# Kernel tuning notes

Measured on AMD Instinct MI355X. Metric: run time of the kernel, lower is better.

## Reference

```python
import jax, jax.numpy as jnp
import numpy as np

B, N, C, H = 16, 577, 768, 12
D = C // H
BETA = 1.0
KEEP_RATIO = 0.5


def setup_inputs() -> dict:
    key = jax.random.key(0)
    k0, k1, k2, k3 = jax.random.split(key, 4)
    x = jax.random.normal(k0, (B, N, C), dtype=jnp.float32)
    # UCB visit-count buffer, strictly positive as accumulated counts would be
    ucb_count_score = jax.random.uniform(k1, (H, N), dtype=jnp.float32) * 50.0 + 1.0
    Wqkv = jax.random.normal(k2, (3 * C, C), dtype=jnp.float32) * 0.02
    Wproj = jax.random.normal(k3, (C, C), dtype=jnp.float32) * 0.02
    bproj = jnp.zeros((C,), dtype=jnp.float32)
    counter = 60  # > 50 so pruning path is taken
    return {"x": x, "ucb_count_score": ucb_count_score, "Wqkv": Wqkv,
            "Wproj": Wproj, "bproj": bproj, "counter": counter}


def reference(x, ucb_count_score, Wqkv, Wproj, bproj, counter):
    # UCBAttention.forward with pruning_enabled=True, selection_mode='ucb',
    # ucb_update_enabled=True, exclude_cls=True, dropout=0 (eval).
    Bs, Ns, Cs = x.shape
    scale = D ** -0.5
    k_keep = max(1, int((Ns - 1) * KEEP_RATIO))  # _get_k with keep_ratio

    qkv = (x @ Wqkv.T).reshape(Bs, Ns, 3, H, D).transpose(2, 0, 3, 1, 4)  # [3,B,H,N,D]
    q, k, v = qkv[0], qkv[1], qkv[2]
    attn_scores = jnp.einsum('bhqd,bhkd->bhqk', q, k) * scale
    attn_probs = jax.nn.softmax(attn_scores, axis=-1)  # [B,H,N,N]

    # UCB scores over patches (CLS excluded)
    patch_scores = attn_probs[:, :, :, 1:].mean(axis=2)            # [B,H,N-1]
    expl = BETA * jnp.sqrt(jnp.log(counter + 1.0) / (ucb_count_score[:, 1:] + 1e-6))
    ucb_scores = patch_scores + expl[None, :, :]                   # [B,H,N-1]
    global_ucb = ucb_scores.mean(axis=1)                           # [B,N-1]
    _, topk_rel = jax.lax.top_k(global_ucb, k_keep)                # [B,k]
    kept = topk_rel + 1                                            # token indices

    # keep-vector: CLS (0) always kept; mask[i,j] = kept[i] OR kept[j]
    kv_mask = (jnp.zeros((Bs, Ns), attn_probs.dtype)
               .at[jnp.arange(Bs)[:, None], kept].set(1.0)
               .at[:, 0].set(1.0))                                 # [B,N]
    mask = jnp.maximum(kv_mask[:, None, :, None], kv_mask[:, None, None, :])  # [B,1,N,N]

    pruned = attn_probs * mask
    pruned = pruned / (pruned.sum(axis=-1, keepdims=True) + 1e-8)
    context = jnp.einsum('bhqk,bhkd->bhqd', pruned, v)             # [B,H,N,D]

    out = context.transpose(0, 2, 1, 3).reshape(Bs, Ns, Cs) @ Wproj.T + bproj

    # score_delta: +1/B at each kept token column, broadcast over heads
    delta = jnp.zeros((Ns,), jnp.float32).at[kept.reshape(-1)].add(1.0 / Bs)
    score_delta = jnp.broadcast_to(delta[None, :], ucb_count_score.shape)
    return out, score_delta, kept
```

## Files before the change

### kernel.cpp

```cpp
#include <hip/hip_runtime.h>
#include <cstdio>
#include <cstdint>

#define B_    16
#define N_    577
#define C_    768
#define H_    12
#define D_    64
#define KKEEP 288
#define SCALE 0.125f
#define LOG2E 1.4426950408889634f
#define M_TOT (B_ * N_)
#define NKT   24
#define PLROW ((size_t)N_ * 64)

typedef __bf16 bf16x8_t __attribute__((ext_vector_type(8)));
typedef __bf16 bf16x4_t __attribute__((ext_vector_type(4)));
typedef float  f32x4_t  __attribute__((ext_vector_type(4)));
typedef unsigned int u32x4_t __attribute__((ext_vector_type(4)));
typedef unsigned int u32x2_t __attribute__((ext_vector_type(2)));

__device__ __forceinline__ f32x4_t mfma_bf16(bf16x8_t a, bf16x8_t b, f32x4_t c) {
    return __builtin_amdgcn_mfma_f32_16x16x32_bf16(a, b, c, 0, 0, 0);
}

__device__ __forceinline__ void gload16(const ushort* g, ushort* l) {
    __builtin_amdgcn_global_load_lds(
        (const __attribute__((address_space(1))) void*)g,
        (__attribute__((address_space(3))) void*)l, 16, 0, 0);
}
#define VMCNT(n) asm volatile("s_waitcnt vmcnt(" #n ")" ::: "memory")
#define LGKM0()  asm volatile("s_waitcnt lgkmcnt(0)" ::: "memory")
#define SB() __builtin_amdgcn_sched_barrier(0)

__device__ __forceinline__ int xcd_swz(int bid, int nwg) {
    int q = nwg >> 3, r = nwg & 7;
    int xcd = bid & 7, off = bid >> 3;
    int base = (xcd < r) ? xcd * (q + 1) : r * (q + 1) + (xcd - r) * q;
    return base + off;
}

__device__ __forceinline__ void splitf(float x, unsigned int &hi, unsigned int &lo) {
    unsigned int u = __float_as_uint(x);
    hi = u >> 16;
    float r = x - __uint_as_float(u & 0xffff0000u);
    lo = __float_as_uint(r) >> 16;
}
__device__ __forceinline__ unsigned int bf16rne(float x) {
    unsigned int u = __float_as_uint(x);
    return (u + 0x7fffu + ((u >> 16) & 1u)) >> 16;
}

__global__ __launch_bounds__(256) void pack_tiles_kernel(const float* __restrict__ src,
                                                         ushort* __restrict__ dH,
                                                         ushort* __restrict__ dL,
                                                         int nrows) {
    int tile = blockIdx.x;
    int kt = tile % NKT, mt = tile / NKT;
    int w = threadIdx.x;
    int row = w >> 1, h = w & 1;
    int m = mt * 128 + row;
    int sw = (row >> 1) & 3;
    float f[16];
    if (m < nrows) {
        const float* s = src + (size_t)m * C_ + kt * 32;
        int sa = (2 * h) ^ sw, sb = (2 * h + 1) ^ sw;
        *(float4*)&f[0]  = *(const float4*)(s + sa * 8);
        *(float4*)&f[4]  = *(const float4*)(s + sa * 8 + 4);
        *(float4*)&f[8]  = *(const float4*)(s + sb * 8);
        *(float4*)&f[12] = *(const float4*)(s + sb * 8 + 4);
    } else {
#pragma unroll
        for (int i = 0; i < 16; i++) f[i] = 0.f;
    }
    unsigned hi[16], lo[16];
#pragma unroll
    for (int i = 0; i < 16; i++) splitf(f[i], hi[i], lo[i]);
    u32x4_t h0 = {hi[0] | (hi[1] << 16), hi[2] | (hi[3] << 16),
                  hi[4] | (hi[5] << 16), hi[6] | (hi[7] << 16)};
    u32x4_t h1 = {hi[8] | (hi[9] << 16), hi[10] | (hi[11] << 16),
                  hi[12] | (hi[13] << 16), hi[14] | (hi[15] << 16)};
    u32x4_t l0 = {lo[0] | (lo[1] << 16), lo[2] | (lo[3] << 16),
                  lo[4] | (lo[5] << 16), lo[6] | (lo[7] << 16)};
    u32x4_t l1 = {lo[8] | (lo[9] << 16), lo[10] | (lo[11] << 16),
                  lo[12] | (lo[13] << 16), lo[14] | (lo[15] << 16)};
    size_t dbase = (size_t)tile * 4096 + row * 32;
    *(u32x4_t*)&dH[dbase + (2 * h) * 8]     = h0;
    *(u32x4_t*)&dH[dbase + (2 * h + 1) * 8] = h1;
    *(u32x4_t*)&dL[dbase + (2 * h) * 8]     = l0;
    *(u32x4_t*)&dL[dbase + (2 * h + 1) * 8] = l1;
}

__global__ __launch_bounds__(256) void pack_rne_kernel(const float* __restrict__ src,
                                                       ushort* __restrict__ dst, int n8) {
    int i = blockIdx.x * 256 + threadIdx.x;
    if (i >= n8) return;
    float4 f0 = ((const float4*)src)[2 * i];
    float4 f1 = ((const float4*)src)[2 * i + 1];
    u32x4_t o = {bf16rne(f0.x) | (bf16rne(f0.y) << 16),
                 bf16rne(f0.z) | (bf16rne(f0.w) << 16),
                 bf16rne(f1.x) | (bf16rne(f1.y) << 16),
                 bf16rne(f1.z) | (bf16rne(f1.w) << 16)};
    *(u32x4_t*)&dst[(size_t)i * 8] = o;
}

__device__ __forceinline__ bf16x8_t fragT(const ushort* H, int row, int c, int ls) {
    int phys = ((c << 2) + ls) ^ (row & 7);
    return __builtin_bit_cast(bf16x8_t, *(const u32x4_t*)&H[(row << 6) + (phys << 3)]);
}

__global__ __launch_bounds__(256) void gemm_qk_mfma(const ushort* __restrict__ XplH,
                                                    const ushort* __restrict__ XplL,
                                                    const ushort* __restrict__ WplH,
                                                    const ushort* __restrict__ WplL,
                                                    ushort* __restrict__ qhp,
                                                    ushort* __restrict__ qlp,
                                                    ushort* __restrict__ khp,
                                                    ushort* __restrict__ klp) {
    __shared__ ushort SMEM[32768];
    ushort* Ah = SMEM;
    ushort* Al = SMEM + 8192;
    ushort* Bh = SMEM + 16384;
    ushort* Bl = SMEM + 24576;
    const int bid = xcd_swz(blockIdx.x, 12 * 73);
    const int bx = bid % 12, by = bid / 12;
    const int tid = threadIdx.x;
    const int lane = tid & 63, wave = tid >> 6;
    const int wr = wave >> 1, wc = wave & 1;
    const int lr = lane & 15, ls = lane >> 4;
    const int m0 = by * 128, n0 = bx * 128;
    const int s = n0 / C_;
    const int o0 = wave * 1024, o1 = o0 + 512;
    const int la = lane * 8;
    const size_t abase = (size_t)by * NKT * 4096;
    const size_t bbase = (size_t)bx * NKT * 4096;
    f32x4_t acc[4][4] = {};

    auto stage = [&](int buf, int kt) {
        const size_t ta = abase + (size_t)kt * 4096;
        const size_t tb = bbase + (size_t)kt * 4096;
        gload16(XplH + ta + o0 + la, &Ah[buf * 4096 + o0]);
        gload16(XplH + ta + o1 + la, &Ah[buf * 4096 + o1]);
        gload16(XplL + ta + o0 + la, &Al[buf * 4096 + o0]);
        gload16(XplL + ta + o1 + la, &Al[buf * 4096 + o1]);
        gload16(WplH + tb + o0 + la, &Bh[buf * 4096 + o0]);
        gload16(WplH + tb + o1 + la, &Bh[buf * 4096 + o1]);
        gload16(WplL + tb + o0 + la, &Bl[buf * 4096 + o0]);
        gload16(WplL + tb + o1 + la, &Bl[buf * 4096 + o1]);
    };
    stage(0, 0);
#pragma unroll 1
    for (int kt = 0; kt < NKT; ++kt) {
        const int cur = kt & 1;
        if (kt + 1 < NKT) {
            stage(cur ^ 1, kt + 1);
            VMCNT(8);
        } else {
            VMCNT(0);
        }
        SB();
        __builtin_amdgcn_s_barrier();
        SB();
        bf16x8_t fah[4], fal[4], fbh[4], fbl[4];
#pragma unroll
        for (int i = 0; i < 4; i++) {
            int rowA = wr * 64 + i * 16 + lr;
            int pa = ls ^ ((rowA >> 1) & 3);
            fah[i] = __builtin_bit_cast(bf16x8_t, *(const u32x4_t*)&Ah[cur * 4096 + rowA * 32 + pa * 8]);
            fal[i] = __builtin_bit_cast(bf16x8_t, *(const u32x4_t*)&Al[cur * 4096 + rowA * 32 + pa * 8]);
            int rowB = wc * 64 + i * 16 + lr;
            int pb = ls ^ ((rowB >> 1) & 3);
            fbh[i] = __builtin_bit_cast(bf16x8_t, *(const u32x4_t*)&Bh[cur * 4096 + rowB * 32 + pb * 8]);
            fbl[i] = __builtin_bit_cast(bf16x8_t, *(const u32x4_t*)&Bl[cur * 4096 + rowB * 32 + pb * 8]);
        }
#pragma unroll
        for (int i = 0; i < 4; i++)
#pragma unroll
            for (int j = 0; j < 4; j++) {
                acc[i][j] = mfma_bf16(fah[i], fbh[j], acc[i][j]);
                acc[i][j] = mfma_bf16(fah[i], fbl[j], acc[i][j]);
                acc[i][j] = mfma_bf16(fal[i], fbh[j], acc[i][j]);
            }
        if (kt + 1 < NKT) {
            SB();
            __builtin_amdgcn_s_barrier();
        }
    }
    __syncthreads();
    unsigned* T = (unsigned*)SMEM;
    const float sc = (s == 0) ? SCALE * LOG2E : 1.0f;
#pragma unroll
    for (int j = 0; j < 4; j++) {
        int nl = wc * 64 + j * 16 + lr;
#pragma unroll
        for (int i = 0; i < 4; i++) {
#pragma unroll
            for (int r = 0; r < 4; r++) {
                int ml = wr * 64 + i * 16 + ls * 4 + r;
                unsigned hi, lo;
                splitf(acc[i][j][r] * sc, hi, lo);
                int idx = ml * 128 + ((((nl >> 3) ^ (ml & 7)) << 3) | (nl & 7));
                T[idx] = hi | (lo << 16);
            }
        }
    }
    __syncthreads();
    ushort* dh = (s == 1) ? khp : qhp;
    ushort* dl = (s == 1) ? klp : qlp;
    const int hh0 = (n0 % C_) / D_;
#pragma unroll
    for (int it = 0; it < 8; ++it) {
        int g = it * 256 + tid;
        int sl = g & 7;
        int m_local = (g >> 3) & 127;
        int hh_half = g >> 10;
        int m = m0 + m_local;
        if (m < M_TOT) {
            int b = m / N_, n = m % N_;
            int dg = sl ^ (n & 7);
            int grp = (hh_half * 8 + dg) ^ (m_local & 7);
            const unsigned* src = &T[m_local * 128 + grp * 8];
            u32x4_t a = *(const u32x4_t*)src;
            u32x4_t bvv = *(const u32x4_t*)(src + 4);
            u32x4_t hiv = {(a[0] & 0xffffu) | (a[1] << 16),
                           (a[2] & 0xffffu) | (a[3] << 16),
                           (bvv[0] & 0xffffu) | (bvv[1] << 16),
                           (bvv[2] & 0xffffu) | (bvv[3] << 16)};
            u32x4_t lov = {(a[0] >> 16) | (a[1] & 0xffff0000u),
                           (a[2] >> 16) | (a[3] & 0xffff0000u),
                           (bvv[0] >> 16) | (bvv[1] & 0xffff0000u),
                           (bvv[2] >> 16) | (bvv[3] & 0xffff0000u)};
            size_t off = (size_t)(b * H_ + hh0 + hh_half) * PLROW + (size_t)n * 64 + sl * 8;
            *(u32x4_t*)&dh[off] = hiv;
            *(u32x4_t*)&dl[off] = lov;
        }
    }
}

__global__ __launch_bounds__(256) void gemm_v_mfma(const ushort* __restrict__ XplH,
                                                   const ushort* __restrict__ XplL,
                                                   const ushort* __restrict__ WplH,
                                                   ushort* __restrict__ vtp) {
    __shared__ ushort Ah[2][4096], Al[2][4096], Bh[2][4096];
    const int bid = xcd_swz(blockIdx.x, 6 * 73);
    const int bx = bid % 6, by = bid / 6;
    const int tid = threadIdx.x;
    const int lane = tid & 63, wave = tid >> 6;
    const int wr = wave >> 1, wc = wave & 1;
    const int lr = lane & 15, ls = lane >> 4;
    const int m0 = by * 128, n0v = bx * 128;
    const int o0 = wave * 1024, o1 = o0 + 512;
    const int la = lane * 8;
    const size_t abase = (size_t)by * NKT * 4096;
    const size_t bbase = (size_t)(12 + bx) * NKT * 4096;
    f32x4_t acc[4][4] = {};

    auto stage = [&](int buf, int kt) {
        const size_t ta = abase + (size_t)kt * 4096;
        const size_t tb = bbase + (size_t)kt * 4096;
        gload16(XplH + ta + o0 + la, &Ah[buf][o0]);
        gload16(XplH + ta + o1 + la, &Ah[buf][o1]);
        gload16(XplL + ta + o0 + la, &Al[buf][o0]);
        gload16(XplL + ta + o1 + la, &Al[buf][o1]);
        gload16(WplH + tb + o0 + la, &Bh[buf][o0]);
        gload16(WplH + tb + o1 + la, &Bh[buf][o1]);
    };
    stage(0, 0);
#pragma unroll 1
    for (int kt = 0; kt < NKT; ++kt) {
        const int cur = kt & 1;
        if (kt + 1 < NKT) {
            stage(cur ^ 1, kt + 1);
            VMCNT(6);
        } else {
            VMCNT(0);
        }
        SB();
        __builtin_amdgcn_s_barrier();
        SB();
        bf16x8_t fah[4], fal[4], fbh[4];
#pragma unroll
        for (int i = 0; i < 4; i++) {
            int rowA = wr * 64 + i * 16 + lr;
            int pa = ls ^ ((rowA >> 1) & 3);
            fah[i] = __builtin_bit_cast(bf16x8_t, *(const u32x4_t*)&Ah[cur][rowA * 32 + pa * 8]);
            fal[i] = __builtin_bit_cast(bf16x8_t, *(const u32x4_t*)&Al[cur][rowA * 32 + pa * 8]);
            int rowB = wc * 64 + i * 16 + lr;
            int pb = ls ^ ((rowB >> 1) & 3);
            fbh[i] = __builtin_bit_cast(bf16x8_t, *(const u32x4_t*)&Bh[cur][rowB * 32 + pb * 8]);
        }
#pragma unroll
        for (int i = 0; i < 4; i++)
#pragma unroll
            for (int j = 0; j < 4; j++) {
                acc[i][j] = mfma_bf16(fah[i], fbh[j], acc[i][j]);
                acc[i][j] = mfma_bf16(fal[i], fbh[j], acc[i][j]);
            }
        if (kt + 1 < NKT) {
            SB();
            __builtin_amdgcn_s_barrier();
        }
    }
#pragma unroll
    for (int j = 0; j < 4; j++) {
        int ng = n0v + wc * 64 + j * 16 + lr;
        int hh = ng / D_;
        int d = ng % D_;
#pragma unroll
        for (int i = 0; i < 4; i++) {
            int mg0 = m0 + wr * 64 + i * 16 + ls * 4;
#pragma unroll
            for (int r = 0; r < 4; r++) {
                int m = mg0 + r;
                if (m < M_TOT) {
                    int b = m / N_, n = m % N_;
                    int jt = n >> 6, jl = n & 63;
                    size_t off = ((size_t)(b * H_ + hh) * 10 + jt) * 4096 +
                                 (size_t)d * 64 + (((jl >> 3) ^ (d & 7)) << 3) + (jl & 7);
                    vtp[off] = __builtin_bit_cast(unsigned short, (__bf16)acc[i][j][r]);
                }
            }
        }
    }
}

__global__ __launch_bounds__(512) void attn_rowsum_mfma(const ushort* __restrict__ qh,
                                                        const ushort* __restrict__ ql,
                                                        const ushort* __restrict__ kh,
                                                        const ushort* __restrict__ kl,
                                                        float* __restrict__ w) {
    __shared__ ushort Qh[8192], Ql[8192];
    __shared__ ushort Kh[4096], Kl[4096];
    __shared__ float red[8][64];
    const int bid = xcd_swz(blockIdx.x, 5 * B_ * H_);
    const int bh = bid / 5, q0 = (bid % 5) * 128;
    const int tid = threadIdx.x, lane = tid & 63, wv = tid >> 6;
    const int wg = wv >> 2, wl = wv & 3;
    const int lr = lane & 15, ls = lane >> 4;
    const size_t bho = (size_t)bh * PLROW;
    const ushort* qhp = qh + bho; const ushort* qlp = ql + bho;
    const ushort* khp = kh + bho; const ushort* klp = kl + bho;
    auto qrow = [&](int rr) { return (size_t)min(q0 + wv * 16 + rr * 8 + (lane >> 3), N_ - 1) * 64 + (lane & 7) * 8; };
    gload16(qhp + qrow(0), &Qh[wv * 1024]);
    gload16(qhp + qrow(1), &Qh[wv * 1024 + 512]);
    gload16(qlp + qrow(0), &Ql[wv * 1024]);
    gload16(qlp + qrow(1), &Ql[wv * 1024 + 512]);
    auto krow = [&](int j0) { return (size_t)min(j0 + wv * 8 + (lane >> 3), N_ - 1) * 64 + (lane & 7) * 8; };
    auto stageK = [&](int j0) {
        gload16(khp + krow(j0), &Kh[wv * 512]);
        gload16(klp + krow(j0), &Kl[wv * 512]);
    };
    stageK(0);
    VMCNT(0);
    __syncthreads();
    bf16x8_t fqh[4][2], fql[4][2];
#pragma unroll
    for (int i = 0; i < 4; i++)
#pragma unroll
        for (int c = 0; c < 2; c++) {
            fqh[i][c] = fragT(Qh, wg * 64 + i * 16 + lr, c, ls);
            fql[i][c] = fragT(Ql, wg * 64 + i * 16 + lr, c, ls);
        }
    float rs[4] = {0.f, 0.f, 0.f, 0.f};
#pragma unroll 1
    for (int t = 0; t < 10; ++t) {
        bf16x8_t fkh[2], fkl[2];
#pragma unroll
        for (int c = 0; c < 2; c++) {
            fkh[c] = fragT(Kh, wl * 16 + lr, c, ls);
            fkl[c] = fragT(Kl, wl * 16 + lr, c, ls);
        }
        int jbase = t * 64 + wl * 16 + ls * 4;
#pragma unroll
        for (int i = 0; i < 4; i++) {
            f32x4_t s = {0.f, 0.f, 0.f, 0.f};
            __builtin_amdgcn_s_setprio(1);
#pragma unroll
            for (int c = 0; c < 2; c++) {
                s = mfma_bf16(fkh[c], fqh[i][c], s);
                s = mfma_bf16(fkh[c], fql[i][c], s);
                s = mfma_bf16(fkl[c], fqh[i][c], s);
            }
            __builtin_amdgcn_s_setprio(0);
#pragma unroll
            for (int r = 0; r < 4; r++)
                rs[i] += (jbase + r < N_) ? __builtin_amdgcn_exp2f(s[r]) : 0.f;
        }
        if (t < 9) {
            SB(); __builtin_amdgcn_s_barrier(); SB();
            stageK((t + 1) * 64);
            VMCNT(0);
            SB(); __builtin_amdgcn_s_barrier(); SB();
        }
    }
#pragma unroll
    for (int i = 0; i < 4; i++) {
        float v2 = rs[i];
        v2 += __shfl_xor(v2, 16);
        v2 += __shfl_xor(v2, 32);
        if (ls == 0) red[wv][i * 16 + lr] = v2;
    }
    __syncthreads();
    if (tid < 128) {
        int grp = tid >> 6, qlc = tid & 63;
        float s = red[grp * 4 + 0][qlc] + red[grp * 4 + 1][qlc] +
                  red[grp * 4 + 2][qlc] + red[grp * 4 + 3][qlc];
        int qn = q0 + tid;
        if (qn < N_) w[(size_t)bh * N_ + qn] = 1.0f / s;
    }
}

__global__ __launch_bounds__(512) void attn_colsum_mfma(const ushort* __restrict__ qh,
                                                        const ushort* __restrict__ ql,
                                                        const ushort* __restrict__ kh,
                                                        const ushort* __restrict__ kl,
                                                        const float* __restrict__ w,
                                                        float* __restrict__ colsum) {
    __shared__ ushort KhS[8192], KlS[8192];
    __shared__ ushort Qh[4096], Ql[4096];
    __shared__ float wsAll[640];
    __shared__ float red[8][64];
    const int bid = xcd_swz(blockIdx.x, 5 * B_ * H_);
    const int bh = bid / 5, j0 = (bid % 5) * 128;
    const int tid = threadIdx.x, lane = tid & 63, wv = tid >> 6;
    const int wg = wv >> 2, wl = wv & 3;
    const int lr = lane & 15, ls = lane >> 4;
    const size_t bho = (size_t)bh * PLROW;
    const ushort* qhp = qh + bho; const ushort* qlp = ql + bho;
    const ushort* khp = kh + bho; const ushort* klp = kl + bho;
    auto krow = [&](int rr) { return (size_t)min(j0 + wv * 16 + rr * 8 + (lane >> 3), N_ - 1) * 64 + (lane & 7) * 8; };
    gload16(khp + krow(0), &KhS[wv * 1024]);
    gload16(khp + krow(1), &KhS[wv * 1024 + 512]);
    gload16(klp + krow(0), &KlS[wv * 1024]);
    gload16(klp + krow(1), &KlS[wv * 1024 + 512]);
    auto qrow2 = [&](int qt) { return (size_t)min(qt + wv * 8 + (lane >> 3), N_ - 1) * 64 + (lane & 7) * 8; };
    auto stageQ = [&](int qt) {
        gload16(qhp + qrow2(qt), &Qh[wv * 512]);
        gload16(qlp + qrow2(qt), &Ql[wv * 512]);
    };
    stageQ(0);
    for (int i2 = tid; i2 < 640; i2 += 512)
        wsAll[i2] = (i2 < N_) ? w[(size_t)bh * N_ + i2] : 0.f;
    VMCNT(0);
    __syncthreads();
    bf16x8_t fkh[4][2], fkl[4][2];
#pragma unroll
    for (int i = 0; i < 4; i++)
#pragma unroll
        for (int c = 0; c < 2; c++) {
            fkh[i][c] = fragT(KhS, wg * 64 + i * 16 + lr, c, ls);
            fkl[i][c] = fragT(KlS, wg * 64 + i * 16 + lr, c, ls);
        }
    float cs[4] = {0.f, 0.f, 0.f, 0.f};
#pragma unroll 1
    for (int t = 0; t < 10; ++t) {
        bf16x8_t fqh[2], fql[2];
#pragma unroll
        for (int c = 0; c < 2; c++) {
            fqh[c] = fragT(Qh, wl * 16 + lr, c, ls);
            fql[c] = fragT(Ql, wl * 16 + lr, c, ls);
        }
        float wq[4];
#pragma unroll
        for (int r = 0; r < 4; r++) wq[r] = wsAll[t * 64 + wl * 16 + ls * 4 + r];
#pragma unroll
        for (int i = 0; i < 4; i++) {
            f32x4_t s = {0.f, 0.f, 0.f, 0.f};
            __builtin_amdgcn_s_setprio(1);
#pragma unroll
            for (int c = 0; c < 2; c++) {
                s = mfma_bf16(fqh[c], fkh[i][c], s);
                s = mfma_bf16(fql[c], fkh[i][c], s);
                s = mfma_bf16(fqh[c], fkl[i][c], s);
            }
            __builtin_amdgcn_s_setprio(0);
#pragma unroll
            for (int r = 0; r < 4; r++) cs[i] += __builtin_amdgcn_exp2f(s[r]) * wq[r];
        }
        if (t < 9) {
            SB(); __builtin_amdgcn_s_barrier(); SB();
            stageQ((t + 1) * 64);
            VMCNT(0);
            SB(); __builtin_amdgcn_s_barrier(); SB();
        }
    }
#pragma unroll
    for (int i = 0; i < 4; i++) {
        float v2 = cs[i];
        v2 += __shfl_xor(v2, 16);
        v2 += __shfl_xor(v2, 32);
        if (ls == 0) red[wv][i * 16 + lr] = v2;
    }
    __syncthreads();
    if (tid < 128) {
        int grp = tid >> 6, jlc = tid & 63;
        float t2 = red[grp * 4 + 0][jlc] + red[grp * 4 + 1][jlc] +
                   red[grp * 4 + 2][jlc] + red[grp * 4 + 3][jlc];
        int jn = j0 + tid;
        if (jn < N_) colsum[(size_t)bh * N_ + jn] = t2;
    }
}

__global__ __launch_bounds__(512) void topk_kernel(const float* __restrict__ colsum,
                                                   const float* __restrict__ ucb_count,
                                                   const int* __restrict__ counter,
                                                   float* __restrict__ kept_out,
                                                   float* __restrict__ kvmask) {
    __shared__ float sv[1024];
    __shared__ int si[1024];
    int b = blockIdx.x, tid = threadIdx.x;
    float lc = logf((float)counter[0] + 1.0f);
    for (int t = tid; t < 1024; t += 512) {
        if (t < N_ - 1) {
            int tok = t + 1;
            float accv = 0.f;
#pragma unroll
            for (int h = 0; h < H_; h++) {
                float csv = colsum[(size_t)(b * H_ + h) * N_ + tok];
                float patch = csv * (1.0f / (float)N_);
                float cnt = ucb_count[h * N_ + tok];
                float expl = sqrtf(lc / (cnt + 1e-6f));
                accv += patch + expl;
            }
            sv[t] = accv * (1.0f / (float)H_);
            si[t] = t;
        } else {
            sv[t] = -INFINITY;
            si[t] = 1 << 20;
        }
    }
    __syncthreads();
    for (int kk = 2; kk <= 1024; kk <<= 1) {
        for (int jj = kk >> 1; jj > 0; jj >>= 1) {
            for (int t = tid; t < 1024; t += 512) {
                int ixj = t ^ jj;
                if (ixj > t) {
                    float v1 = sv[t], v2 = sv[ixj];
                    int i1 = si[t], i2 = si[ixj];
                    bool before21 = (v2 > v1) || (v2 == v1 && i2 < i1);
                    bool dirDesc = ((t & kk) == 0);
                    if (before21 == dirDesc) {
                        sv[t] = v2; sv[ixj] = v1;
                        si[t] = i2; si[ixj] = i1;
                    }
                }
            }
            __syncthreads();
        }
    }
    for (int r = tid; r < KKEEP; r += 512) {
        int tok = si[r] + 1;
        kept_out[b * KKEEP + r] = (float)tok;
        kvmask[b * N_ + tok] = 1.0f;
    }
    if (tid == 0) kvmask[b * N_] = 1.0f;
}

__global__ void score_delta_kernel(const float* __restrict__ kvmask,
                                   float* __restrict__ sd) {
    int idx = blockIdx.x * 256 + threadIdx.x;
    if (idx >= H_ * N_) return;
    int n = idx % N_;
    float d = 0.f;
    if (n != 0) {
#pragma unroll
        for (int b = 0; b < B_; b++) d += kvmask[b * N_ + n];
    }
    sd[idx] = d * (1.0f / (float)B_);
}

__global__ __launch_bounds__(512) void attn_ctx_mfma(const ushort* __restrict__ qh,
                                                     const ushort* __restrict__ ql,
                                                     const ushort* __restrict__ kh,
                                                     const ushort* __restrict__ vtp,
                                                     const float* __restrict__ kvmask,
                                                     ushort* __restrict__ ctxb) {
    __shared__ ushort Kh[2][4096], Vt[2][4096];
    __shared__ ushort Pl[2][4096];
    __shared__ float mkAll[640];
    float (*red)[64] = (float(*)[64])&Pl[0][0];
    float* inv = (float*)&Pl[1][0];
    const int bid = xcd_swz(blockIdx.x, 5 * B_ * H_);
    const int bh = bid / 5, q0 = (bid % 5) * 128;
    const int b = bh / H_, h = bh % H_;
    const int tid = threadIdx.x, lane = tid & 63, wv = tid >> 6;
    const int wg = wv >> 2, wl = wv & 3;
    const int lr = lane & 15, ls = lane >> 4;
    const size_t bho = (size_t)bh * PLROW;
    const ushort* qhp = qh + bho; const ushort* qlp = ql + bho;
    const ushort* khp = kh + bho;
    const ushort* vtb = vtp + (size_t)bh * 10 * 4096;
    ushort* PlS = &Pl[0][0];
    for (int i2 = tid; i2 < 640; i2 += 512)
        mkAll[i2] = (i2 < N_) ? kvmask[(size_t)b * N_ + i2] : 0.f;
    auto qrow = [&](int rr) { return (size_t)min(q0 + wv * 16 + rr * 8 + (lane >> 3), N_ - 1) * 64 + (lane & 7) * 8; };
    bf16x8_t fqh[4][2], fql[4][2];
    gload16(qhp + qrow(0), &PlS[wv * 1024]);
    gload16(qhp + qrow(1), &PlS[wv * 1024 + 512]);
    VMCNT(0); __syncthreads();
#pragma unroll
    for (int i = 0; i < 4; i++)
#pragma unroll
        for (int c = 0; c < 2; c++)
            fqh[i][c] = fragT(PlS, wg * 64 + i * 16 + lr, c, ls);
    __syncthreads();
    gload16(qlp + qrow(0), &PlS[wv * 1024]);
    gload16(qlp + qrow(1), &PlS[wv * 1024 + 512]);
    VMCNT(0); __syncthreads();
#pragma unroll
    for (int i = 0; i < 4; i++)
#pragma unroll
        for (int c = 0; c < 2; c++)
            fql[i][c] = fragT(PlS, wg * 64 + i * 16 + lr, c, ls);
    __syncthreads();
    auto krow = [&](int j0) { return (size_t)min(j0 + wv * 8 + (lane >> 3), N_ - 1) * 64 + (lane & 7) * 8; };
    auto stageKV = [&](int buf, int t) {
        gload16(khp + krow(t * 64), &Kh[buf][wv * 512]);
        gload16(vtb + (size_t)t * 4096 + wv * 512 + lane * 8, &Vt[buf][wv * 512]);
    };
    float mq[4];
#pragma unroll
    for (int i = 0; i < 4; i++) mq[i] = mkAll[q0 + wg * 64 + i * 16 + lr];
    stageKV(0, 0);
    f32x4_t acc[4] = {};
    float psums[4] = {0.f, 0.f, 0.f, 0.f};
#pragma unroll 1
    for (int t = 0; t < 10; ++t) {
        const int cur = t & 1;
        if (t < 9) { stageKV(cur ^ 1, t + 1); VMCNT(2); }
        else      { VMCNT(0); }
        SB(); __builtin_amdgcn_s_barrier(); SB();
        bf16x8_t fkh[2];
#pragma unroll
        for (int c = 0; c < 2; c++)
            fkh[c] = fragT(Kh[cur], wl * 16 + lr, c, ls);
        int jloc = wl * 16 + ls * 4;
        float jmv[4], jbias[4];
#pragma unroll
        for (int r = 0; r < 4; r++) {
            int j = t * 64 + jloc + r;
            jmv[r] = mkAll[t * 64 + jloc + r];
            jbias[r] = (j < N_) ? 0.f : -16384.f;
        }
#pragma unroll
        for (int i = 0; i < 4; i++) {
            f32x4_t s = {0.f, 0.f, 0.f, 0.f};
            __builtin_amdgcn_s_setprio(1);
#pragma unroll
            for (int c = 0; c < 2; c++) {
                s = mfma_bf16(fkh[c], fqh[i][c], s);
                s = mfma_bf16(fkh[c], fql[i][c], s);
            }
            __builtin_amdgcn_s_setprio(0);
            bf16x4_t pb;
            float mqi = mq[i];
#pragma unroll
            for (int r = 0; r < 4; r++) {
                float p = __builtin_amdgcn_exp2f(s[r] + jbias[r]) * fmaxf(mqi, jmv[r]);
                psums[i] += p;
                pb[r] = (__bf16)p;
            }
            int row = i * 16 + lr;
            int slot = ((wl << 1) + (ls >> 1)) ^ (row & 7);
            *(u32x2_t*)&Pl[wg][(row << 6) + (slot << 3) + ((ls & 1) << 2)] =
                __builtin_bit_cast(u32x2_t, pb);
        }
        SB(); LGKM0(); SB();
        __builtin_amdgcn_s_barrier();
        SB();
        bf16x8_t fv[2];
#pragma unroll
        for (int c = 0; c < 2; c++) fv[c] = fragT(Vt[cur], wl * 16 + lr, c, ls);
        __builtin_amdgcn_s_setprio(1);
#pragma unroll
        for (int i = 0; i < 4; i++) {
            bf16x8_t fp0 = fragT(Pl[wg], i * 16 + lr, 0, ls);
            bf16x8_t fp1 = fragT(Pl[wg], i * 16 + lr, 1, ls);
            acc[i] = mfma_bf16(fv[0], fp0, acc[i]);
            acc[i] = mfma_bf16(fv[1], fp1, acc[i]);
        }
        __builtin_amdgcn_s_setprio(0);
        if (t < 9) { SB(); __builtin_amdgcn_s_barrier(); }
    }
    __syncthreads();
#pragma unroll
    for (int i = 0; i < 4; i++) {
        float v2 = psums[i];
        v2 += __shfl_xor(v2, 16);
        v2 += __shfl_xor(v2, 32);
        if (ls == 0) red[wv][i * 16 + lr] = v2;
    }
    __syncthreads();
    if (tid < 128) {
        int grp = tid >> 6, qlc = tid & 63;
        float t2 = red[grp * 4 + 0][qlc] + red[grp * 4 + 1][qlc] +
                   red[grp * 4 + 2][qlc] + red[grp * 4 + 3][qlc];
        inv[tid] = 1.0f / (t2 + 1e-8f);
    }
    __syncthreads();
#pragma unroll
    for (int i = 0; i < 4; i++) {
        int qn = q0 + wg * 64 + i * 16 + lr;
        if (qn < N_) {
            float rn = inv[wg * 64 + i * 16 + lr];
            bf16x4_t ov;
            ov[0] = (__bf16)(acc[i][0] * rn);
            ov[1] = (__bf16)(acc[i][1] * rn);
            ov[2] = (__bf16)(acc[i][2] * rn);
            ov[3] = (__bf16)(acc[i][3] * rn);
            *(u32x2_t*)&ctxb[((size_t)(b * N_ + qn)) * C_ + h * D_ + wl * 16 + ls * 4] =
                __builtin_bit_cast(u32x2_t, ov);
        }
    }
}

__global__ __launch_bounds__(256) void gemm_proj_mfma(const ushort* __restrict__ Actx,
                                                      const ushort* __restrict__ Wb,
                                                      const float* __restrict__ bias,
                                                      float* __restrict__ out) {
    __shared__ ushort Ab[128 * 32], Bb[128 * 32];
    const int bid = xcd_swz(blockIdx.x, 6 * 73);
    const int bx = bid % 6, by = bid / 6;
    const int tid = threadIdx.x;
    const int lane = tid & 63, wave = tid >> 6;
    const int wr = wave >> 1, wc = wave & 1;
    const int lr = lane & 15, ls = lane >> 4;
    const int m0 = by * 128, n0 = bx * 128;
    const int srow = tid >> 1, shalf = tid & 1;
    const int arow = min(m0 + srow, M_TOT - 1);
    const ushort* aptr = Actx + (size_t)arow * C_ + shalf * 16;
    const ushort* bptr = Wb + (size_t)(n0 + srow) * C_ + shalf * 16;
    const int swz = (srow >> 1) & 3;
    const int sidx = srow * 32;
    const int p0 = (shalf * 2 + 0) ^ swz, p1 = (shalf * 2 + 1) ^ swz;
    f32x4_t acc[4][4] = {};
#pragma unroll 1
    for (int k0 = 0; k0 < C_; k0 += 32) {
        __syncthreads();
        {
            u32x4_t c0 = *(const u32x4_t*)(aptr + k0);
            u32x4_t c1 = *(const u32x4_t*)(aptr + k0 + 8);
            *(u32x4_t*)&Ab[sidx + p0 * 8] = c0;
            *(u32x4_t*)&Ab[sidx + p1 * 8] = c1;
        }
        {
            u32x4_t c0 = *(const u32x4_t*)(bptr + k0);
            u32x4_t c1 = *(const u32x4_t*)(bptr + k0 + 8);
            *(u32x4_t*)&Bb[sidx + p0 * 8] = c0;
            *(u32x4_t*)&Bb[sidx + p1 * 8] = c1;
        }
        __syncthreads();
        bf16x8_t fa[4], fb[4];
#pragma unroll
        for (int i = 0; i < 4; i++) {
            int rowA = wr * 64 + i * 16 + lr;
            int pa = ls ^ ((rowA >> 1) & 3);
            fa[i] = __builtin_bit_cast(bf16x8_t, *(const u32x4_t*)&Ab[rowA * 32 + pa * 8]);
            int rowB = wc * 64 + i * 16 + lr;
            int pb = ls ^ ((rowB >> 1) & 3);
            fb[i] = __builtin_bit_cast(bf16x8_t, *(const u32x4_t*)&Bb[rowB * 32 + pb * 8]);
        }
#pragma unroll
        for (int i = 0; i < 4; i++)
#pragma unroll
            for (int j = 0; j < 4; j++)
                acc[i][j] = mfma_bf16(fa[i], fb[j], acc[i][j]);
    }
#pragma unroll
    for (int j = 0; j < 4; j++) {
        int ng = n0 + wc * 64 + j * 16 + lr;
        float bb = bias[ng];
#pragma unroll
        for (int i = 0; i < 4; i++) {
            int mg0 = m0 + wr * 64 + i * 16 + ls * 4;
#pragma unroll
            for (int r = 0; r < 4; r++) {
                int m = mg0 + r;
                if (m < M_TOT) out[(size_t)m * C_ + ng] = acc[i][j][r] + bb;
            }
        }
    }
}

extern "C" void kernel_launch(void* const* d_in, const int* in_sizes, int n_in,
                              void* d_out, int out_size, void* d_ws, size_t ws_size,
                              hipStream_t stream) {
    const float* x     = (const float*)d_in[0];
    const float* ucb   = (const float*)d_in[1];
    const float* Wqkv  = (const float*)d_in[2];
    const float* Wproj = (const float*)d_in[3];
    const float* bproj = (const float*)d_in[4];
    const int*   counter = (const int*)d_in[5];

    const size_t BHN  = (size_t)B_ * H_ * N_;
    const size_t XPL  = (size_t)(73 * 128) * C_;
    const size_t WPL  = (size_t)3 * C_ * C_;
    const size_t WPJ  = (size_t)C_ * C_;
    const size_t PLN  = (size_t)192 * PLROW;
    const size_t VTSZ = (size_t)192 * 10 * 4096;

    ushort* qhp  = (ushort*)d_ws;
    ushort* qlp  = qhp + PLN;
    ushort* khp  = qlp + PLN;
    ushort* klp  = khp + PLN;
    ushort* vtp  = klp + PLN;
    ushort* XplH = vtp + VTSZ;
    ushort* XplL = XplH + XPL;
    ushort* ctxb = XplH;
    ushort* WplH = XplL + XPL;
    ushort* WplL = WplH + WPL;
    ushort* Wpjb = WplL + WPL;
    float*  w    = (float*)(Wpjb + WPJ);
    float*  colsum = w + BHN;
    float*  kvmask = colsum + BHN;
    size_t need = ((char*)(kvmask + (size_t)B_ * N_)) - (char*)d_ws;
    if (ws_size < need) {
        fprintf(stderr, "kernel_launch: ws too small, need %zu have %zu\n",
                need, ws_size);
        return;
    }

    float* out  = (float*)d_out;
    float* sd   = out + (size_t)B_ * N_ * C_;
    float* kept = sd + (size_t)H_ * N_;

    hipMemsetAsync(kvmask, 0, (size_t)B_ * N_ * sizeof(float), stream);

    pack_tiles_kernel<<<73 * NKT, 256, 0, stream>>>(x, XplH, XplL, M_TOT);
    pack_tiles_kernel<<<18 * NKT, 256, 0, stream>>>(Wqkv, WplH, WplL, 3 * C_);
    pack_rne_kernel<<<(int)(WPJ / 8 / 256), 256, 0, stream>>>(Wproj, Wpjb, (int)(WPJ / 8));

    gemm_qk_mfma<<<12 * 73, 256, 0, stream>>>(XplH, XplL, WplH, WplL,
                                              qhp, qlp, khp, klp);
    gemm_v_mfma<<<6 * 73, 256, 0, stream>>>(XplH, XplL, WplH, vtp);
    attn_rowsum_mfma<<<5 * B_ * H_, 512, 0, stream>>>(qhp, qlp, khp, klp, w);
    attn_colsum_mfma<<<5 * B_ * H_, 512, 0, stream>>>(qhp, qlp, khp, klp, w, colsum);
    topk_kernel<<<B_, 512, 0, stream>>>(colsum, ucb, counter, kept, kvmask);
    score_delta_kernel<<<(H_ * N_ + 255) / 256, 256, 0, stream>>>(kvmask, sd);
    attn_ctx_mfma<<<5 * B_ * H_, 512, 0, stream>>>(qhp, qlp, khp, vtp,
                                                   kvmask, ctxb);
    gemm_proj_mfma<<<6 * 73, 256, 0, stream>>>(ctxb, Wpjb, bproj, out);
}
```

Measured before the change: 310.5 us.

## Merge pack, memset, QKV GEMMs and score-delta launches into fewer kernels

Folds the two tile-pack kernels, the Wproj bf16 pack and the kvmask memset into one pack_all kernel. The separate QK and V GEMMs become a single gemm_qkv launch that branches on the column tile, and score_delta now runs as extra blocks of attn_ctx. The aim is fewer launches and gaps between kernels, and letting the V tiles fill the GPU alongside the QK tiles. It also changes the LDS swizzle in the Q/K epilogue transpose, which may alter bank conflicts. The fused GEMM kernel carries the register and LDS needs of both paths.

```diff
diff --git a/kernel.cpp b/kernel.cpp
--- a/kernel.cpp
+++ b/kernel.cpp
@@ -51,11 +51,10 @@
     return (u + 0x7fffu + ((u >> 16) & 1u)) >> 16;
 }
 
-__global__ __launch_bounds__(256) void pack_tiles_kernel(const float* __restrict__ src,
-                                                         ushort* __restrict__ dH,
-                                                         ushort* __restrict__ dL,
-                                                         int nrows) {
-    int tile = blockIdx.x;
+__device__ __forceinline__ void pack_tile(const float* __restrict__ src,
+                                          ushort* __restrict__ dH,
+                                          ushort* __restrict__ dL,
+                                          int nrows, int tile) {
     int kt = tile % NKT, mt = tile / NKT;
     int w = threadIdx.x;
     int row = w >> 1, h = w & 1;
@@ -91,17 +90,38 @@
     *(u32x4_t*)&dL[dbase + (2 * h + 1) * 8] = l1;
 }
 
-__global__ __launch_bounds__(256) void pack_rne_kernel(const float* __restrict__ src,
-                                                       ushort* __restrict__ dst, int n8) {
-    int i = blockIdx.x * 256 + threadIdx.x;
-    if (i >= n8) return;
-    float4 f0 = ((const float4*)src)[2 * i];
-    float4 f1 = ((const float4*)src)[2 * i + 1];
-    u32x4_t o = {bf16rne(f0.x) | (bf16rne(f0.y) << 16),
-                 bf16rne(f0.z) | (bf16rne(f0.w) << 16),
-                 bf16rne(f1.x) | (bf16rne(f1.y) << 16),
-                 bf16rne(f1.z) | (bf16rne(f1.w) << 16)};
-    *(u32x4_t*)&dst[(size_t)i * 8] = o;
+#define NXP 1752
+#define NWP 432
+#define NRNE 288
+#define NZ  37
+
+__global__ __launch_bounds__(256) void pack_all_kernel(const float* __restrict__ x,
+                                                       const float* __restrict__ Wqkv,
+                                                       const float* __restrict__ Wproj,
+                                                       ushort* __restrict__ XplH,
+                                                       ushort* __restrict__ XplL,
+                                                       ushort* __restrict__ WplH,
+                                                       ushort* __restrict__ WplL,
+                                                       ushort* __restrict__ Wpjb,
+                                                       float* __restrict__ kvmask) {
+    int bid = blockIdx.x;
+    if (bid < NXP) {
+        pack_tile(x, XplH, XplL, M_TOT, bid);
+    } else if (bid < NXP + NWP) {
+        pack_tile(Wqkv, WplH, WplL, 3 * C_, bid - NXP);
+    } else if (bid < NXP + NWP + NRNE) {
+        int i = (bid - NXP - NWP) * 256 + threadIdx.x;
+        float4 f0 = ((const float4*)Wproj)[2 * i];
+        float4 f1 = ((const float4*)Wproj)[2 * i + 1];
+        u32x4_t o = {bf16rne(f0.x) | (bf16rne(f0.y) << 16),
+                     bf16rne(f0.z) | (bf16rne(f0.w) << 16),
+                     bf16rne(f1.x) | (bf16rne(f1.y) << 16),
+                     bf16rne(f1.z) | (bf16rne(f1.w) << 16)};
+        *(u32x4_t*)&Wpjb[(size_t)i * 8] = o;
+    } else {
+        int i = (bid - NXP - NWP - NRNE) * 256 + threadIdx.x;
+        if (i < B_ * N_) kvmask[i] = 0.f;
+    }
 }
 
 __device__ __forceinline__ bf16x8_t fragT(const ushort* H, int row, int c, int ls) {
@@ -109,215 +129,201 @@
     return __builtin_bit_cast(bf16x8_t, *(const u32x4_t*)&H[(row << 6) + (phys << 3)]);
 }
 
-__global__ __launch_bounds__(256) void gemm_qk_mfma(const ushort* __restrict__ XplH,
-                                                    const ushort* __restrict__ XplL,
-                                                    const ushort* __restrict__ WplH,
-                                                    const ushort* __restrict__ WplL,
-                                                    ushort* __restrict__ qhp,
-                                                    ushort* __restrict__ qlp,
-                                                    ushort* __restrict__ khp,
-                                                    ushort* __restrict__ klp) {
+__global__ __launch_bounds__(256) void gemm_qkv_mfma(const ushort* __restrict__ XplH,
+                                                     const ushort* __restrict__ XplL,
+                                                     const ushort* __restrict__ WplH,
+                                                     const ushort* __restrict__ WplL,
+                                                     ushort* __restrict__ qhp,
+                                                     ushort* __restrict__ qlp,
+                                                     ushort* __restrict__ khp,
+                                                     ushort* __restrict__ klp,
+                                                     ushort* __restrict__ vtp) {
     __shared__ ushort SMEM[32768];
     ushort* Ah = SMEM;
     ushort* Al = SMEM + 8192;
     ushort* Bh = SMEM + 16384;
     ushort* Bl = SMEM + 24576;
-    const int bid = xcd_swz(blockIdx.x, 12 * 73);
-    const int bx = bid % 12, by = bid / 12;
+    const int bid = xcd_swz(blockIdx.x, 18 * 73);
+    const int bx = bid % 18, by = bid / 18;
     const int tid = threadIdx.x;
     const int lane = tid & 63, wave = tid >> 6;
     const int wr = wave >> 1, wc = wave & 1;
     const int lr = lane & 15, ls = lane >> 4;
-    const int m0 = by * 128, n0 = bx * 128;
-    const int s = n0 / C_;
+    const int m0 = by * 128;
     const int o0 = wave * 1024, o1 = o0 + 512;
     const int la = lane * 8;
     const size_t abase = (size_t)by * NKT * 4096;
     const size_t bbase = (size_t)bx * NKT * 4096;
     f32x4_t acc[4][4] = {};
 
-    auto stage = [&](int buf, int kt) {
-        const size_t ta = abase + (size_t)kt * 4096;
-        const size_t tb = bbase + (size_t)kt * 4096;
-        gload16(XplH + ta + o0 + la, &Ah[buf * 4096 + o0]);
-        gload16(XplH + ta + o1 + la, &Ah[buf * 4096 + o1]);
-        gload16(XplL + ta + o0 + la, &Al[buf * 4096 + o0]);
-        gload16(XplL + ta + o1 + la, &Al[buf * 4096 + o1]);
-        gload16(WplH + tb + o0 + la, &Bh[buf * 4096 + o0]);
-        gload16(WplH + tb + o1 + la, &Bh[buf * 4096 + o1]);
-        gload16(WplL + tb + o0 + la, &Bl[buf * 4096 + o0]);
-        gload16(WplL + tb + o1 + la, &Bl[buf * 4096 + o1]);
-    };
-    stage(0, 0);
+    if (bx < 12) {
+        auto stage = [&](int buf, int kt) {
+            const size_t ta = abase + (size_t)kt * 4096;
+            const size_t tb = bbase + (size_t)kt * 4096;
+            gload16(XplH + ta + o0 + la, &Ah[buf * 4096 + o0]);
+            gload16(XplH + ta + o1 + la, &Ah[buf * 4096 + o1]);
+            gload16(XplL + ta + o0 + la, &Al[buf * 4096 + o0]);
+            gload16(XplL + ta + o1 + la, &Al[buf * 4096 + o1]);
+            gload16(WplH + tb + o0 + la, &Bh[buf * 4096 + o0]);
+            gload16(WplH + tb + o1 + la, &Bh[buf * 4096 + o1]);
+            gload16(WplL + tb + o0 + la, &Bl[buf * 4096 + o0]);
+            gload16(WplL + tb + o1 + la, &Bl[buf * 4096 + o1]);
+        };
+        stage(0, 0);
 #pragma unroll 1
-    for (int kt = 0; kt < NKT; ++kt) {
-        const int cur = kt & 1;
-        if (kt + 1 < NKT) {
-            stage(cur ^ 1, kt + 1);
-            VMCNT(8);
-        } else {
-            VMCNT(0);
-        }
-        SB();
-        __builtin_amdgcn_s_barrier();
-        SB();
-        bf16x8_t fah[4], fal[4], fbh[4], fbl[4];
-#pragma unroll
-        for (int i = 0; i < 4; i++) {
-            int rowA = wr * 64 + i * 16 + lr;
-            int pa = ls ^ ((rowA >> 1) & 3);
-            fah[i] = __builtin_bit_cast(bf16x8_t, *(const u32x4_t*)&Ah[cur * 4096 + rowA * 32 + pa * 8]);
-            fal[i] = __builtin_bit_cast(bf16x8_t, *(const u32x4_t*)&Al[cur * 4096 + rowA * 32 + pa * 8]);
-            int rowB = wc * 64 + i * 16 + lr;
-            int pb = ls ^ ((rowB >> 1) & 3);
-            fbh[i] = __builtin_bit_cast(bf16x8_t, *(const u32x4_t*)&Bh[cur * 4096 + rowB * 32 + pb * 8]);
-            fbl[i] = __builtin_bit_cast(bf16x8_t, *(const u32x4_t*)&Bl[cur * 4096 + rowB * 32 + pb * 8]);
-        }
-#pragma unroll
-        for (int i = 0; i < 4; i++)
-#pragma unroll
-            for (int j = 0; j < 4; j++) {
-                acc[i][j] = mfma_bf16(fah[i], fbh[j], acc[i][j]);
-                acc[i][j] = mfma_bf16(fah[i], fbl[j], acc[i][j]);
-                acc[i][j] = mfma_bf16(fal[i], fbh[j], acc[i][j]);
-            }
-        if (kt + 1 < NKT) {
+        for (int kt = 0; kt < NKT; ++kt) {
+            const int cur = kt & 1;
+            if (kt + 1 < NKT) {
+                stage(cur ^ 1, kt + 1);
+                VMCNT(8);
+            } else {
+                VMCNT(0);
+            }
             SB();
             __builtin_amdgcn_s_barrier();
-        }
-    }
-    __syncthreads();
-    unsigned* T = (unsigned*)SMEM;
-    const float sc = (s == 0) ? SCALE * LOG2E : 1.0f;
-#pragma unroll
-    for (int j = 0; j < 4; j++) {
-        int nl = wc * 64 + j * 16 + lr;
-#pragma unroll
-        for (int i = 0; i < 4; i++) {
-#pragma unroll
-            for (int r = 0; r < 4; r++) {
-                int ml = wr * 64 + i * 16 + ls * 4 + r;
-                unsigned hi, lo;
-                splitf(acc[i][j][r] * sc, hi, lo);
-                int idx = ml * 128 + ((((nl >> 3) ^ (ml & 7)) << 3) | (nl & 7));
-                T[idx] = hi | (lo << 16);
-            }
-        }
-    }
-    __syncthreads();
-    ushort* dh = (s == 1) ? khp : qhp;
-    ushort* dl = (s == 1) ? klp : qlp;
-    const int hh0 = (n0 % C_) / D_;
-#pragma unroll
-    for (int it = 0; it < 8; ++it) {
-        int g = it * 256 + tid;
-        int sl = g & 7;
-        int m_local = (g >> 3) & 127;
-        int hh_half = g >> 10;
-        int m = m0 + m_local;
-        if (m < M_TOT) {
-            int b = m / N_, n = m % N_;
-            int dg = sl ^ (n & 7);
-            int grp = (hh_half * 8 + dg) ^ (m_local & 7);
-            const unsigned* src = &T[m_local * 128 + grp * 8];
-            u32x4_t a = *(const u32x4_t*)src;
-            u32x4_t bvv = *(const u32x4_t*)(src + 4);
-            u32x4_t hiv = {(a[0] & 0xffffu) | (a[1] << 16),
-                           (a[2] & 0xffffu) | (a[3] << 16),
-                           (bvv[0] & 0xffffu) | (bvv[1] << 16),
-                           (bvv[2] & 0xffffu) | (bvv[3] << 16)};
-            u32x4_t lov = {(a[0] >> 16) | (a[1] & 0xffff0000u),
-                           (a[2] >> 16) | (a[3] & 0xffff0000u),
-                           (bvv[0] >> 16) | (bvv[1] & 0xffff0000u),
-                           (bvv[2] >> 16) | (bvv[3] & 0xffff0000u)};
-            size_t off = (size_t)(b * H_ + hh0 + hh_half) * PLROW + (size_t)n * 64 + sl * 8;
-            *(u32x4_t*)&dh[off] = hiv;
-            *(u32x4_t*)&dl[off] = lov;
-        }
-    }
-}
-
-__global__ __launch_bounds__(256) void gemm_v_mfma(const ushort* __restrict__ XplH,
-                                                   const ushort* __restrict__ XplL,
-                                                   const ushort* __restrict__ WplH,
-                                                   ushort* __restrict__ vtp) {
-    __shared__ ushort Ah[2][4096], Al[2][4096], Bh[2][4096];
-    const int bid = xcd_swz(blockIdx.x, 6 * 73);
-    const int bx = bid % 6, by = bid / 6;
-    const int tid = threadIdx.x;
-    const int lane = tid & 63, wave = tid >> 6;
-    const int wr = wave >> 1, wc = wave & 1;
-    const int lr = lane & 15, ls = lane >> 4;
-    const int m0 = by * 128, n0v = bx * 128;
-    const int o0 = wave * 1024, o1 = o0 + 512;
-    const int la = lane * 8;
-    const size_t abase = (size_t)by * NKT * 4096;
-    const size_t bbase = (size_t)(12 + bx) * NKT * 4096;
-    f32x4_t acc[4][4] = {};
-
-    auto stage = [&](int buf, int kt) {
-        const size_t ta = abase + (size_t)kt * 4096;
-        const size_t tb = bbase + (size_t)kt * 4096;
-        gload16(XplH + ta + o0 + la, &Ah[buf][o0]);
-        gload16(XplH + ta + o1 + la, &Ah[buf][o1]);
-        gload16(XplL + ta + o0 + la, &Al[buf][o0]);
-        gload16(XplL + ta + o1 + la, &Al[buf][o1]);
-        gload16(WplH + tb + o0 + la, &Bh[buf][o0]);
-        gload16(WplH + tb + o1 + la, &Bh[buf][o1]);
-    };
-    stage(0, 0);
+            SB();
+            bf16x8_t fah[4], fal[4], fbh[4], fbl[4];
+#pragma unroll
+            for (int i = 0; i < 4; i++) {
+                int rowA = wr * 64 + i * 16 + lr;
+                int pa = ls ^ ((rowA >> 1) & 3);
+                fah[i] = __builtin_bit_cast(bf16x8_t, *(const u32x4_t*)&Ah[cur * 4096 + rowA * 32 + pa * 8]);
+                fal[i] = __builtin_bit_cast(bf16x8_t, *(const u32x4_t*)&Al[cur * 4096 + rowA * 32 + pa * 8]);
+                int rowB = wc * 64 + i * 16 + lr;
+                int pb = ls ^ ((rowB >> 1) & 3);
+                fbh[i] = __builtin_bit_cast(bf16x8_t, *(const u32x4_t*)&Bh[cur * 4096 + rowB * 32 + pb * 8]);
+                fbl[i] = __builtin_bit_cast(bf16x8_t, *(const u32x4_t*)&Bl[cur * 4096 + rowB * 32 + pb * 8]);
+            }
+#pragma unroll
+            for (int i = 0; i < 4; i++)
+#pragma unroll
+                for (int j = 0; j < 4; j++) {
+                    acc[i][j] = mfma_bf16(fah[i], fbh[j], acc[i][j]);
+                    acc[i][j] = mfma_bf16(fah[i], fbl[j], acc[i][j]);
+                    acc[i][j] = mfma_bf16(fal[i], fbh[j], acc[i][j]);
+                }
+            if (kt + 1 < NKT) {
+                SB();
+                __builtin_amdgcn_s_barrier();
+            }
+        }
+        const int n0 = bx * 128;
+        const int s = n0 / C_;
+        __syncthreads();
+        unsigned* T = (unsigned*)SMEM;
+        const float sc = (s == 0) ? SCALE * LOG2E : 1.0f;
+#pragma unroll
+        for (int j = 0; j < 4; j++) {
+            int nl = wc * 64 + j * 16 + lr;
+#pragma unroll
+            for (int i = 0; i < 4; i++) {
+#pragma unroll
+                for (int r = 0; r < 4; r++) {
+                    int ml = wr * 64 + i * 16 + ls * 4 + r;
+                    unsigned hi, lo;
+                    splitf(acc[i][j][r] * sc, hi, lo);
+                    int idx = ml * 128 + ((((nl >> 3) ^ ((ml >> 2) & 7)) << 3) | (nl & 7));
+                    T[idx] = hi | (lo << 16);
+                }
+            }
+        }
+        __syncthreads();
+        ushort* dh = (s == 1) ? khp : qhp;
+        ushort* dl = (s == 1) ? klp : qlp;
+        const int hh0 = (n0 % C_) / D_;
+#pragma unroll
+        for (int it = 0; it < 8; ++it) {
+            int g = it * 256 + tid;
+            int sl = g & 7;
+            int m_local = (g >> 3) & 127;
+            int hh_half = g >> 10;
+            int m = m0 + m_local;
+            if (m < M_TOT) {
+                int b = m / N_, n = m % N_;
+                int dg = sl ^ (n & 7);
+                int grp = (hh_half * 8 + dg) ^ ((m_local >> 2) & 7);
+                const unsigned* src = &T[m_local * 128 + grp * 8];
+                u32x4_t a = *(const u32x4_t*)src;
+                u32x4_t bvv = *(const u32x4_t*)(src + 4);
+                u32x4_t hiv = {(a[0] & 0xffffu) | (a[1] << 16),
+                               (a[2] & 0xffffu) | (a[3] << 16),
+                               (bvv[0] & 0xffffu) | (bvv[1] << 16),
+                               (bvv[2] & 0xffffu) | (bvv[3] << 16)};
+                u32x4_t lov = {(a[0] >> 16) | (a[1] & 0xffff0000u),
+                               (a[2] >> 16) | (a[3] & 0xffff0000u),
+                               (bvv[0] >> 16) | (bvv[1] & 0xffff0000u),
+                               (bvv[2] >> 16) | (bvv[3] & 0xffff0000u)};
+                size_t off = (size_t)(b * H_ + hh0 + hh_half) * PLROW + (size_t)n * 64 + sl * 8;
+                *(u32x4_t*)&dh[off] = hiv;
+                *(u32x4_t*)&dl[off] = lov;
+            }
+        }
+    } else {
+        auto stage = [&](int buf, int kt) {
+            const size_t ta = abase + (size_t)kt * 4096;
+            const size_t tb = bbase + (size_t)kt * 4096;
+            gload16(XplH + ta + o0 + la, &Ah[buf * 4096 + o0]);
+            gload16(XplH + ta + o1 + la, &Ah[buf * 4096 + o1]);
+            gload16(XplL + ta + o0 + la, &Al[buf * 4096 + o0]);
+            gload16(XplL + ta + o1 + la, &Al[buf * 4096 + o1]);
+            gload16(WplH + tb + o0 + la, &Bh[buf * 4096 + o0]);
+            gload16(WplH + tb + o1 + la, &Bh[buf * 4096 + o1]);
+        };
+        stage(0, 0);
 #pragma unroll 1
-    for (int kt = 0; kt < NKT; ++kt) {
-        const int cur = kt & 1;
-        if (kt + 1 < NKT) {
-            stage(cur ^ 1, kt + 1);
-            VMCNT(6);
-        } else {
-            VMCNT(0);
-        }
-        SB();
-        __builtin_amdgcn_s_barrier();
-        SB();
-        bf16x8_t fah[4], fal[4], fbh[4];
-#pragma unroll
-        for (int i = 0; i < 4; i++) {
-            int rowA = wr * 64 + i * 16 + lr;
-            int pa = ls ^ ((rowA >> 1) & 3);
-            fah[i] = __builtin_bit_cast(bf16x8_t, *(const u32x4_t*)&Ah[cur][rowA * 32 + pa * 8]);
-            fal[i] = __builtin_bit_cast(bf16x8_t, *(const u32x4_t*)&Al[cur][rowA * 32 + pa * 8]);
-            int rowB = wc * 64 + i * 16 + lr;
-            int pb = ls ^ ((rowB >> 1) & 3);
-            fbh[i] = __builtin_bit_cast(bf16x8_t, *(const u32x4_t*)&Bh[cur][rowB * 32 + pb * 8]);
-        }
-#pragma unroll
-        for (int i = 0; i < 4; i++)
-#pragma unroll
-            for (int j = 0; j < 4; j++) {
-                acc[i][j] = mfma_bf16(fah[i], fbh[j], acc[i][j]);
-                acc[i][j] = mfma_bf16(fal[i], fbh[j], acc[i][j]);
-            }
-        if (kt + 1 < NKT) {
+        for (int kt = 0; kt < NKT; ++kt) {
+            const int cur = kt & 1;
+            if (kt + 1 < NKT) {
+                stage(cur ^ 1, kt + 1);
+                VMCNT(6);
+            } else {
+                VMCNT(0);
+            }
             SB();
             __builtin_amdgcn_s_barrier();
-        }
-    }
-#pragma unroll
-    for (int j = 0; j < 4; j++) {
-        int ng = n0v + wc * 64 + j * 16 + lr;
-        int hh = ng / D_;
-        int d = ng % D_;
-#pragma unroll
-        for (int i = 0; i < 4; i++) {
-            int mg0 = m0 + wr * 64 + i * 16 + ls * 4;
-#pragma unroll
-            for (int r = 0; r < 4; r++) {
-                int m = mg0 + r;
-                if (m < M_TOT) {
-                    int b = m / N_, n = m % N_;
-                    int jt = n >> 6, jl = n & 63;
-                    size_t off = ((size_t)(b * H_ + hh) * 10 + jt) * 4096 +
-                                 (size_t)d * 64 + (((jl >> 3) ^ (d & 7)) << 3) + (jl & 7);
-                    vtp[off] = __builtin_bit_cast(unsigned short, (__bf16)acc[i][j][r]);
+            SB();
+            bf16x8_t fah[4], fal[4], fbh[4];
+#pragma unroll
+            for (int i = 0; i < 4; i++) {
+                int rowA = wr * 64 + i * 16 + lr;
+                int pa = ls ^ ((rowA >> 1) & 3);
+                fah[i] = __builtin_bit_cast(bf16x8_t, *(const u32x4_t*)&Ah[cur * 4096 + rowA * 32 + pa * 8]);
+                fal[i] = __builtin_bit_cast(bf16x8_t, *(const u32x4_t*)&Al[cur * 4096 + rowA * 32 + pa * 8]);
+                int rowB = wc * 64 + i * 16 + lr;
+                int pb = ls ^ ((rowB >> 1) & 3);
+                fbh[i] = __builtin_bit_cast(bf16x8_t, *(const u32x4_t*)&Bh[cur * 4096 + rowB * 32 + pb * 8]);
+            }
+#pragma unroll
+            for (int i = 0; i < 4; i++)
+#pragma unroll
+                for (int j = 0; j < 4; j++) {
+                    acc[i][j] = mfma_bf16(fah[i], fbh[j], acc[i][j]);
+                    acc[i][j] = mfma_bf16(fal[i], fbh[j], acc[i][j]);
+                }
+            if (kt + 1 < NKT) {
+                SB();
+                __builtin_amdgcn_s_barrier();
+            }
+        }
+        const int n0v = (bx - 12) * 128;
+#pragma unroll
+        for (int j = 0; j < 4; j++) {
+            int ng = n0v + wc * 64 + j * 16 + lr;
+            int hh = ng / D_;
+            int d = ng % D_;
+#pragma unroll
+            for (int i = 0; i < 4; i++) {
+                int mg0 = m0 + wr * 64 + i * 16 + ls * 4;
+#pragma unroll
+                for (int r = 0; r < 4; r++) {
+                    int m = mg0 + r;
+                    if (m < M_TOT) {
+                        int b = m / N_, n = m % N_;
+                        int jt = n >> 6, jl = n & 63;
+                        size_t off = ((size_t)(b * H_ + hh) * 10 + jt) * 4096 +
+                                     (size_t)d * 64 + (((jl >> 3) ^ (d & 7)) << 3) + (jl & 7);
+                        vtp[off] = __builtin_bit_cast(unsigned short, (__bf16)acc[i][j][r]);
+                    }
                 }
             }
         }
@@ -556,25 +562,26 @@
     if (tid == 0) kvmask[b * N_] = 1.0f;
 }
 
-__global__ void score_delta_kernel(const float* __restrict__ kvmask,
-                                   float* __restrict__ sd) {
-    int idx = blockIdx.x * 256 + threadIdx.x;
-    if (idx >= H_ * N_) return;
-    int n = idx % N_;
-    float d = 0.f;
-    if (n != 0) {
-#pragma unroll
-        for (int b = 0; b < B_; b++) d += kvmask[b * N_ + n];
-    }
-    sd[idx] = d * (1.0f / (float)B_);
-}
-
 __global__ __launch_bounds__(512) void attn_ctx_mfma(const ushort* __restrict__ qh,
                                                      const ushort* __restrict__ ql,
                                                      const ushort* __restrict__ kh,
                                                      const ushort* __restrict__ vtp,
                                                      const float* __restrict__ kvmask,
-                                                     ushort* __restrict__ ctxb) {
+                                                     ushort* __restrict__ ctxb,
+                                                     float* __restrict__ sd) {
+    if (blockIdx.x >= 5 * B_ * H_) {
+        int idx = (blockIdx.x - 5 * B_ * H_) * 512 + threadIdx.x;
+        if (idx < H_ * N_) {
+            int n = idx % N_;
+            float d = 0.f;
+            if (n != 0) {
+#pragma unroll
+                for (int b = 0; b < B_; b++) d += kvmask[b * N_ + n];
+            }
+            sd[idx] = d * (1.0f / (float)B_);
+        }
+        return;
+    }
     __shared__ ushort Kh[2][4096], Vt[2][4096];
     __shared__ ushort Pl[2][4096];
     __shared__ float mkAll[640];
@@ -824,20 +831,15 @@
     float* sd   = out + (size_t)B_ * N_ * C_;
     float* kept = sd + (size_t)H_ * N_;
 
-    hipMemsetAsync(kvmask, 0, (size_t)B_ * N_ * sizeof(float), stream);
-
-    pack_tiles_kernel<<<73 * NKT, 256, 0, stream>>>(x, XplH, XplL, M_TOT);
-    pack_tiles_kernel<<<18 * NKT, 256, 0, stream>>>(Wqkv, WplH, WplL, 3 * C_);
-    pack_rne_kernel<<<(int)(WPJ / 8 / 256), 256, 0, stream>>>(Wproj, Wpjb, (int)(WPJ / 8));
-
-    gemm_qk_mfma<<<12 * 73, 256, 0, stream>>>(XplH, XplL, WplH, WplL,
-                                              qhp, qlp, khp, klp);
-    gemm_v_mfma<<<6 * 73, 256, 0, stream>>>(XplH, XplL, WplH, vtp);
+    pack_all_kernel<<<NXP + NWP + NRNE + NZ, 256, 0, stream>>>(
+        x, Wqkv, Wproj, XplH, XplL, WplH, WplL, Wpjb, kvmask);
+
+    gemm_qkv_mfma<<<18 * 73, 256, 0, stream>>>(XplH, XplL, WplH, WplL,
+                                               qhp, qlp, khp, klp, vtp);
     attn_rowsum_mfma<<<5 * B_ * H_, 512, 0, stream>>>(qhp, qlp, khp, klp, w);
     attn_colsum_mfma<<<5 * B_ * H_, 512, 0, stream>>>(qhp, qlp, khp, klp, w, colsum);
     topk_kernel<<<B_, 512, 0, stream>>>(colsum, ucb, counter, kept, kvmask);
-    score_delta_kernel<<<(H_ * N_ + 255) / 256, 256, 0, stream>>>(kvmask, sd);
-    attn_ctx_mfma<<<5 * B_ * H_, 512, 0, stream>>>(qhp, qlp, khp, vtp,
-                                                   kvmask, ctxb);
+    attn_ctx_mfma<<<5 * B_ * H_ + 14, 512, 0, stream>>>(qhp, qlp, khp, vtp,
+                                                        kvmask, ctxb, sd);
     gemm_proj_mfma<<<6 * 73, 256, 0, stream>>>(ctxb, Wpjb, bproj, out);
 }
```

Measured after the change: 289.6 us. 6.8% less time.
